# Kernel optimization log

Measured on AMD Instinct MI355X. Metric: run time of the kernel, lower is better.

The kernel has to match this reference:

```python
import jax, jax.numpy as jnp
import numpy as np

HEAD_DIM = 64

def setup_inputs() -> dict:
    key = jax.random.key(0)
    k1, k2, k3, k4, k5 = jax.random.split(key, 5)
    T, B, E = 2048, 4, 1024
    KD = 64  # kdim
    x = jax.random.normal(k1, (T, B, E), dtype=jnp.float32)
    in_proj_weight = jax.random.normal(k2, (3 * KD, HEAD_DIM), dtype=jnp.float32) * (1.0 / np.sqrt(HEAD_DIM))
    in_proj_bias = jnp.zeros((3 * KD,), dtype=jnp.float32)
    out_w = jax.random.normal(k4, (HEAD_DIM, KD), dtype=jnp.float32) * (1.0 / np.sqrt(KD))
    out_b = jnp.zeros((HEAD_DIM,), dtype=jnp.float32)
    return {"x": x, "in_proj_weight": in_proj_weight, "in_proj_bias": in_proj_bias,
            "out_w": out_w, "out_b": out_b}

def reference(x, in_proj_weight, in_proj_bias, out_w, out_b):
    # x: [T, B, E] with E = H * HEAD_DIM (qkv_same self-attention path)
    T, B, E = x.shape
    H = E // HEAD_DIM
    KD = in_proj_weight.shape[0] // 3
    scaling = HEAD_DIM ** (-0.5)
    # reshape splits embed dim into heads: [T, B*H, 64]
    xh = x.reshape(T, B * H, HEAD_DIM)
    # fused in-projection: [T, B*H, 3*KD], then chunk into q/k/v
    qkv = xh @ in_proj_weight.T + in_proj_bias
    q, k, v = jnp.split(qkv, 3, axis=-1)          # each [T, B*H, KD]
    q = q * scaling
    q = q.transpose(1, 0, 2)                      # [B*H, T, KD]
    k = k.transpose(1, 0, 2)
    v = v.transpose(1, 0, 2)
    scores = jnp.einsum('btd,bsd->bts', q, k)     # [B*H, T, T]
    w = jax.nn.softmax(scores, axis=-1)
    attn = jnp.einsum('bts,bsd->btd', w, v)       # [B*H, T, KD]
    attn = attn.transpose(1, 0, 2).reshape(T, B, H, KD)
    out = attn @ out_w.T + out_b                  # [T, B, H, HEAD_DIM]
    out = out.reshape(T, B, H * HEAD_DIM)         # [T, B, E]
    # averaged attention weights over heads: [B, T, T]
    avg_w = w.reshape(B, H, T, T).sum(axis=1) / H
    return out, avg_w
```

## Files before the change

kernel.cpp:

```cpp
#include <hip/hip_runtime.h>
#include <hip/hip_bf16.h>

#define T_DIM 2048
#define B_DIM 4
#define E_DIM 1024

typedef __bf16 bf16_t;
typedef bf16_t bf16x8 __attribute__((ext_vector_type(8)));
typedef float f32x16 __attribute__((ext_vector_type(16)));

union frag_u { uint4 u; bf16x8 b; };

constexpr float SCALEQ = 0.18033688011112042f;

__device__ __forceinline__ f32x16 mfma32(bf16x8 a, bf16x8 b, f32x16 c) {
  return __builtin_amdgcn_mfma_f32_32x32x16_bf16(a, b, c, 0, 0, 0);
}
__device__ __forceinline__ unsigned packbf(float a, float b) {
  union { bf16_t h[2]; unsigned u; } r;
  r.h[0] = (bf16_t)a; r.h[1] = (bf16_t)b; return r.u;
}
__device__ __forceinline__ void pl32swap(unsigned &x, unsigned &y) {
  asm volatile("v_permlane32_swap_b32 %0, %1" : "+v"(x), "+v"(y));
}
__device__ __forceinline__ void gload16(const void* g, void* l) {
  __builtin_amdgcn_global_load_lds((const __attribute__((address_space(1))) void*)g,
                                   (__attribute__((address_space(3))) void*)l, 16, 0, 0);
}
__device__ __forceinline__ bf16x8 ldc(const char* base, int chunk, int row) {
  frag_u f; f.u = *(const uint4*)(base + chunk * 1024 + row * 16); return f.b;
}
__device__ __forceinline__ float ex2(float x) { return __builtin_amdgcn_exp2f(x); }

#define VMCNT4 asm volatile("s_waitcnt vmcnt(4)" ::: "memory")
#define VMCNT0 asm volatile("s_waitcnt vmcnt(0)" ::: "memory")
#define LGKM0  asm volatile("s_waitcnt lgkmcnt(0)" ::: "memory")

template <int O>
__device__ __forceinline__ uint4 mkfrag(const f32x16& A) {
  unsigned X = packbf(A[O + 0], A[O + 1]);
  unsigned Z = packbf(A[O + 2], A[O + 3]);
  unsigned Y = packbf(A[O + 4], A[O + 5]);
  unsigned W = packbf(A[O + 6], A[O + 7]);
  pl32swap(X, Y); pl32swap(Z, W);
  return (uint4){X, Z, Y, W};
}

__global__ __launch_bounds__(256) void qkv_kernel(
    const float* __restrict__ x, const float* __restrict__ W,
    const float* __restrict__ bias,
    bf16_t* __restrict__ Qc, bf16_t* __restrict__ Kc, bf16_t* __restrict__ Vc) {
  __shared__ __align__(16) char xlds[16384];
  __shared__ __align__(16) char wlds[24576];
  __shared__ float bs[192];
  const int tid = threadIdx.x;
  const int bh = blockIdx.x >> 4;
  const int tt = blockIdx.x & 15;
  const int b = bh >> 4, h = bh & 15;
  const int t0 = tt * 128;
  const int wid = tid >> 6, lane = tid & 63;
  const int lq = lane & 31, hi = lane >> 5;

  for (int i = tid; i < 1024; i += 256) {
    int t = i >> 3, oct = i & 7;
    const float* src = x + ((size_t)(t0 + t) * B_DIM + b) * E_DIM + h * 64 + oct * 8;
    float4 f0 = *(const float4*)src;
    float4 f1 = *(const float4*)(src + 4);
    uint4 u;
    u.x = packbf(f0.x, f0.y); u.y = packbf(f0.z, f0.w);
    u.z = packbf(f1.x, f1.y); u.w = packbf(f1.z, f1.w);
    *(uint4*)(xlds + oct * 2048 + t * 16) = u;
  }
  for (int i = tid; i < 1536; i += 256) {
    int r = i >> 3, oct = i & 7;
    const float* src = W + r * 64 + oct * 8;
    float4 f0 = *(const float4*)src;
    float4 f1 = *(const float4*)(src + 4);
    uint4 u;
    u.x = packbf(f0.x, f0.y); u.y = packbf(f0.z, f0.w);
    u.z = packbf(f1.x, f1.y); u.w = packbf(f1.z, f1.w);
    *(uint4*)(wlds + oct * 3072 + r * 16) = u;
  }
  if (tid < 192) bs[tid] = bias[tid];
  __syncthreads();

  frag_u bx[4];
  #pragma unroll
  for (int s = 0; s < 4; ++s)
    bx[s].u = *(const uint4*)(xlds + (s * 2 + hi) * 2048 + (wid * 32 + lq) * 16);

  f32x16 acc[6];
  #pragma unroll
  for (int mt = 0; mt < 6; ++mt)
    #pragma unroll
    for (int r = 0; r < 16; ++r) acc[mt][r] = 0.f;

  #pragma unroll
  for (int mt = 0; mt < 6; ++mt) {
    #pragma unroll
    for (int s = 0; s < 4; ++s) {
      frag_u aw;
      aw.u = *(const uint4*)(wlds + (s * 2 + hi) * 3072 + (mt * 32 + lq) * 16);
      acc[mt] = mfma32(aw.b, bx[s].b, acc[mt]);
    }
  }

  const size_t tb = ((size_t)bh * 32 + (t0 >> 6) + (wid >> 1)) * 4096;
  const int trow = (wid & 1) * 32 + lq;

  #pragma unroll
  for (int mt = 0; mt < 6; ++mt) {
    #pragma unroll
    for (int g = 0; g < 4; ++g) {
      int rbase = mt * 32 + 8 * g + 4 * hi;
      float4 bq = *(const float4*)&bs[rbase];
      float v0 = acc[mt][4 * g + 0] + bq.x;
      float v1 = acc[mt][4 * g + 1] + bq.y;
      float v2 = acc[mt][4 * g + 2] + bq.z;
      float v3 = acc[mt][4 * g + 3] + bq.w;
      if (mt < 2) {
        union { ushort4 us; unsigned u2[2]; } pk;
        pk.u2[0] = packbf(v0 * SCALEQ, v1 * SCALEQ);
        pk.u2[1] = packbf(v2 * SCALEQ, v3 * SCALEQ);
        int d0 = rbase;
        *(ushort4*)(Qc + tb + (d0 >> 3) * 512 + trow * 8 + (d0 & 7)) = pk.us;
      } else if (mt < 4) {
        union { ushort4 us; unsigned u2[2]; } pk;
        pk.u2[0] = packbf(v0, v1);
        pk.u2[1] = packbf(v2, v3);
        int d0 = rbase - 64;
        *(ushort4*)(Kc + tb + (d0 >> 3) * 512 + trow * 8 + (d0 & 7)) = pk.us;
      } else {
        int d0 = rbase - 128;
        bf16_t* vdst = Vc + tb + (trow >> 3) * 512 + (trow & 7);
        vdst[(size_t)(d0 + 0) * 8] = (bf16_t)v0;
        vdst[(size_t)(d0 + 1) * 8] = (bf16_t)v1;
        vdst[(size_t)(d0 + 2) * 8] = (bf16_t)v2;
        vdst[(size_t)(d0 + 3) * 8] = (bf16_t)v3;
      }
    }
  }
}

__global__ __launch_bounds__(256, 2) void flash_kernel(
    const bf16_t* __restrict__ Qc, const bf16_t* __restrict__ Kc,
    const bf16_t* __restrict__ Vc,
    const float* __restrict__ Wo, const float* __restrict__ bo,
    float* __restrict__ out, float* __restrict__ Lv) {
  __shared__ __align__(16) char lds[32768];
  __shared__ __align__(16) char wlds[8192];
  const int tid = threadIdx.x;
  const int bid = ((blockIdx.x & 7) << 6) | (blockIdx.x >> 3);
  const int bh = bid >> 3, qb = bid & 7;
  const int b = bh >> 4, h = bh & 15;
  const int wid = tid >> 6, lane = tid & 63;
  const int lq = lane & 31, hi = lane >> 5;
  const int q0 = qb * 256 + wid * 64;

  for (int i = tid; i < 512; i += 256) {
    int d = i >> 3, oct = i & 7;
    const float* src = Wo + d * 64 + oct * 8;
    float4 f0 = *(const float4*)src;
    float4 f1 = *(const float4*)(src + 4);
    uint4 u;
    u.x = packbf(f0.x, f0.y); u.y = packbf(f0.z, f0.w);
    u.z = packbf(f1.x, f1.y); u.w = packbf(f1.z, f1.w);
    *(uint4*)(wlds + oct * 1024 + d * 16) = u;
  }

  const bf16_t* qtb = Qc + ((size_t)bh * 32 + (q0 >> 6)) * 4096;
  frag_u qfA[4], qfB[4];
  #pragma unroll
  for (int s = 0; s < 4; ++s) {
    qfA[s].u = *(const uint4*)(qtb + (s * 2 + hi) * 512 + lq * 8);
    qfB[s].u = *(const uint4*)(qtb + (s * 2 + hi) * 512 + (32 + lq) * 8);
  }

  f32x16 oA0, oA1, oB0, oB1;
  #pragma unroll
  for (int i = 0; i < 16; ++i) { oA0[i] = 0.f; oA1[i] = 0.f; oB0[i] = 0.f; oB1[i] = 0.f; }
  float lA = 0.f, lB = 0.f;

  const bf16_t* kbh = Kc + (size_t)bh * 131072;
  const bf16_t* vbh = Vc + (size_t)bh * 131072;
  auto stage = [&](int buf, int t) {
    char* kl_ = lds + buf * 16384 + wid * 2048;
    char* vl_ = kl_ + 8192;
    const bf16_t* kt = kbh + (size_t)t * 4096 + wid * 1024 + lane * 8;
    const bf16_t* vt = vbh + (size_t)t * 4096 + wid * 1024 + lane * 8;
    gload16(kt, kl_); gload16(kt + 512, kl_ + 1024);
    gload16(vt, vl_); gload16(vt + 512, vl_ + 1024);
  };

  stage(0, 0); stage(1, 1);
  VMCNT4; __builtin_amdgcn_sched_barrier(0);
  __builtin_amdgcn_s_barrier();

  for (int t = 0; t < 32; ++t) {
    const char* kl = lds + (t & 1) * 16384;
    const char* vl = kl + 8192;

    bf16x8 k0[4], k1[4];
    #pragma unroll
    for (int s = 0; s < 4; ++s) {
      k0[s] = ldc(kl, s * 2 + hi, lq);
      k1[s] = ldc(kl, s * 2 + hi, 32 + lq);
    }
    f32x16 aA0, aA1, aB0, aB1;
    #pragma unroll
    for (int i = 0; i < 16; ++i) { aA0[i] = 0.f; aA1[i] = 0.f; aB0[i] = 0.f; aB1[i] = 0.f; }
    __builtin_amdgcn_s_setprio(1);
    #pragma unroll
    for (int s = 0; s < 4; ++s) {
      aA0 = mfma32(k0[s], qfA[s].b, aA0);
      aA1 = mfma32(k1[s], qfA[s].b, aA1);
      aB0 = mfma32(k0[s], qfB[s].b, aB0);
      aB1 = mfma32(k1[s], qfB[s].b, aB1);
    }
    __builtin_amdgcn_s_setprio(0);

    bf16x8 v0[4], v1[4];
    #pragma unroll
    for (int s = 0; s < 4; ++s) {
      v0[s] = ldc(vl, s * 2 + hi, lq);
      v1[s] = ldc(vl, s * 2 + hi, 32 + lq);
    }
    LGKM0; __builtin_amdgcn_sched_barrier(0);
    __builtin_amdgcn_s_barrier();
    if (t + 2 < 32) stage(t & 1, t + 2);

    float lsA = 0.f, lsB = 0.f;
    #pragma unroll
    for (int i = 0; i < 16; ++i) {
      aA0[i] = ex2(aA0[i]); aA1[i] = ex2(aA1[i]);
      aB0[i] = ex2(aB0[i]); aB1[i] = ex2(aB1[i]);
      lsA += aA0[i] + aA1[i]; lsB += aB0[i] + aB1[i];
    }
    lA += lsA; lB += lsB;

    frag_u pA[4], pB[4];
    pA[0].u = mkfrag<0>(aA0); pA[1].u = mkfrag<8>(aA0);
    pA[2].u = mkfrag<0>(aA1); pA[3].u = mkfrag<8>(aA1);
    pB[0].u = mkfrag<0>(aB0); pB[1].u = mkfrag<8>(aB0);
    pB[2].u = mkfrag<0>(aB1); pB[3].u = mkfrag<8>(aB1);

    __builtin_amdgcn_s_setprio(1);
    #pragma unroll
    for (int ks = 0; ks < 4; ++ks) {
      oA0 = mfma32(v0[ks], pA[ks].b, oA0);
      oA1 = mfma32(v1[ks], pA[ks].b, oA1);
      oB0 = mfma32(v0[ks], pB[ks].b, oB0);
      oB1 = mfma32(v1[ks], pB[ks].b, oB1);
    }
    __builtin_amdgcn_s_setprio(0);

    if (t < 30) { VMCNT4; } else { VMCNT0; }
    __builtin_amdgcn_sched_barrier(0);
    __builtin_amdgcn_s_barrier();
  }

  float ltA = lA + __shfl_xor(lA, 32);
  float ltB = lB + __shfl_xor(lB, 32);
  float iA = 1.f / ltA, iB = 1.f / ltB;
  #pragma unroll
  for (int i = 0; i < 16; ++i) { oA0[i] *= iA; oA1[i] *= iA; oB0[i] *= iB; oB1[i] *= iB; }

  frag_u fA[4], fB[4];
  fA[0].u = mkfrag<0>(oA0); fA[1].u = mkfrag<8>(oA0);
  fA[2].u = mkfrag<0>(oA1); fA[3].u = mkfrag<8>(oA1);
  fB[0].u = mkfrag<0>(oB0); fB[1].u = mkfrag<8>(oB0);
  fB[2].u = mkfrag<0>(oB1); fB[3].u = mkfrag<8>(oB1);

  f32x16 cA0, cA1, cB0, cB1;
  #pragma unroll
  for (int i = 0; i < 16; ++i) { cA0[i] = 0.f; cA1[i] = 0.f; cB0[i] = 0.f; cB1[i] = 0.f; }
  #pragma unroll
  for (int s = 0; s < 4; ++s) {
    frag_u w0, w1;
    w0.u = *(const uint4*)(wlds + (s * 2 + hi) * 1024 + lq * 16);
    w1.u = *(const uint4*)(wlds + (s * 2 + hi) * 1024 + (32 + lq) * 16);
    cA0 = mfma32(fA[s].b, w0.b, cA0);
    cA1 = mfma32(fA[s].b, w1.b, cA1);
    cB0 = mfma32(fB[s].b, w0.b, cB0);
    cB1 = mfma32(fB[s].b, w1.b, cB1);
  }
  float bo0 = bo[lq], bo1 = bo[32 + lq];
  #pragma unroll
  for (int r = 0; r < 16; ++r) {
    int trA = q0 + (r & 3) + 8 * (r >> 2) + 4 * hi;
    int trB = trA + 32;
    out[((size_t)trA * B_DIM + b) * E_DIM + h * 64 + lq]      = cA0[r] + bo0;
    out[((size_t)trA * B_DIM + b) * E_DIM + h * 64 + 32 + lq] = cA1[r] + bo1;
    out[((size_t)trB * B_DIM + b) * E_DIM + h * 64 + lq]      = cB0[r] + bo0;
    out[((size_t)trB * B_DIM + b) * E_DIM + h * 64 + 32 + lq] = cB1[r] + bo1;
  }
  if (lane < 32) {
    Lv[(size_t)bh * T_DIM + q0 + lane] = ltA;
    Lv[(size_t)bh * T_DIM + q0 + 32 + lane] = ltB;
  }
}

__global__ __launch_bounds__(256, 2) void avgw_kernel(
    const bf16_t* __restrict__ Qc, const bf16_t* __restrict__ Kc,
    const float* __restrict__ Lv, float* __restrict__ avgw) {
  __shared__ __align__(16) char qlds[2][16384];
  __shared__ __align__(16) char klds[2][16384];
  __shared__ float lw[16][128];
  const int tid = threadIdx.x;
  const int bid = ((blockIdx.x & 7) << 7) | (blockIdx.x >> 3);
  const int b = bid >> 8, tq = (bid >> 4) & 15, sq = bid & 15;
  const int t0 = tq * 128, s0 = sq * 128;
  const int wid = tid >> 6, lane = tid & 63;
  const int lq = lane & 31, hi = lane >> 5;
  const int wr = wid >> 1, wc = wid & 1;

  for (int i = tid; i < 2048; i += 256) {
    int h = i >> 7, tt = i & 127;
    size_t idx = ((size_t)(b * 16 + h)) * T_DIM + t0 + tt;
    lw[h >> 3][0] = lw[h >> 3][0];
    lw[h][tt] = 1.0f / (16.0f * Lv[idx]);
  }

  auto stage = [&](int buf, int h) {
    int bh = b * 16 + h;
    const bf16_t* qt = Qc + ((size_t)bh * 32 + (t0 >> 6)) * 4096;
    const bf16_t* kt = Kc + ((size_t)bh * 32 + (s0 >> 6)) * 4096;
    #pragma unroll
    for (int j = 0; j < 4; ++j) {
      gload16(qt + wid * 2048 + j * 512 + lane * 8, qlds[buf] + wid * 4096 + j * 1024);
      gload16(kt + wid * 2048 + j * 512 + lane * 8, klds[buf] + wid * 4096 + j * 1024);
    }
  };

  f32x16 sacc[2][2];
  #pragma unroll
  for (int i = 0; i < 2; ++i)
    #pragma unroll
    for (int j = 0; j < 2; ++j)
      #pragma unroll
      for (int r = 0; r < 16; ++r) sacc[i][j][r] = 0.f;

  stage(0, 0);
  __syncthreads();

  for (int h = 0; h < 16; ++h) {
    if (h < 15) stage((h + 1) & 1, h + 1);
    const char* qb = qlds[h & 1];
    const char* kb = klds[h & 1];

    frag_u aq[2][4], ak[2][4];
    #pragma unroll
    for (int i = 0; i < 2; ++i)
      #pragma unroll
      for (int s = 0; s < 4; ++s) {
        int rq = wr * 64 + i * 32 + lq;
        int rk = wc * 64 + i * 32 + lq;
        aq[i][s].u = *(const uint4*)(qb + (rq >> 6) * 8192 + (s * 2 + hi) * 1024 + (rq & 63) * 16);
        ak[i][s].u = *(const uint4*)(kb + (rk >> 6) * 8192 + (s * 2 + hi) * 1024 + (rk & 63) * 16);
      }

    float lwr[2][16];
    #pragma unroll
    for (int i = 0; i < 2; ++i)
      #pragma unroll
      for (int r = 0; r < 16; ++r)
        lwr[i][r] = lw[h][wr * 64 + i * 32 + (r & 3) + ((r >> 2) << 3) + (hi << 2)];

    #pragma unroll
    for (int i = 0; i < 2; ++i)
      #pragma unroll
      for (int j = 0; j < 2; ++j) {
        f32x16 c;
        #pragma unroll
        for (int r = 0; r < 16; ++r) c[r] = 0.f;
        __builtin_amdgcn_s_setprio(1);
        #pragma unroll
        for (int s = 0; s < 4; ++s) c = mfma32(aq[i][s].b, ak[j][s].b, c);
        __builtin_amdgcn_s_setprio(0);
        #pragma unroll
        for (int r = 0; r < 16; ++r) sacc[i][j][r] += ex2(c[r]) * lwr[i][r];
      }
    __syncthreads();
  }

  #pragma unroll
  for (int i = 0; i < 2; ++i)
    #pragma unroll
    for (int j = 0; j < 2; ++j)
      #pragma unroll
      for (int r = 0; r < 16; ++r) {
        int trow = t0 + wr * 64 + i * 32 + (r & 3) + ((r >> 2) << 3) + (hi << 2);
        int scol = s0 + wc * 64 + j * 32 + lq;
        avgw[((size_t)b * T_DIM + trow) * T_DIM + scol] = sacc[i][j][r];
      }
}

extern "C" void kernel_launch(void* const* d_in, const int* in_sizes, int n_in,
                              void* d_out, int out_size, void* d_ws, size_t ws_size,
                              hipStream_t stream) {
  const float* x    = (const float*)d_in[0];
  const float* W    = (const float*)d_in[1];
  const float* bias = (const float*)d_in[2];
  const float* Wo   = (const float*)d_in[3];
  const float* bo   = (const float*)d_in[4];
  float* out  = (float*)d_out;
  float* avgw = out + (size_t)T_DIM * B_DIM * E_DIM;

  char* ws = (char*)d_ws;
  bf16_t* Qc = (bf16_t*)(ws);
  bf16_t* Kc = (bf16_t*)(ws + (16u << 20));
  bf16_t* Vc = (bf16_t*)(ws + (32u << 20));
  float*  Lv = (float*)(ws + (48u << 20));

  qkv_kernel<<<dim3(1024), dim3(256), 0, stream>>>(x, W, bias, Qc, Kc, Vc);
  flash_kernel<<<dim3(512), dim3(256), 0, stream>>>(Qc, Kc, Vc, Wo, bo, out, Lv);
  avgw_kernel<<<dim3(1024), dim3(256), 0, stream>>>(Qc, Kc, Lv, avgw);
}
```

Measured before the change: 178.2 us.

## Split flash attention KV sequence across waves with LDS reduction of partial outputs

The flash kernel now gives each block 64 queries instead of 256, and each of the four waves handles a quarter of the key/value sequence with its own private double-buffered LDS stage. Partial outputs and row sums are reduced through LDS, and the waves then split the output projection. This removes per-iteration block barriers and raises the grid from 512 to 2048 blocks for better occupancy and load balance. The cost is that every block rereads Wo, a larger LDS footprint (64KB) that may limit blocks per CU, and the extra reduction pass. MFMA chains now start from a zero constant instead of zeroing accumulators first.

```diff
diff --git a/kernel.cpp b/kernel.cpp
--- a/kernel.cpp
+++ b/kernel.cpp
@@ -7,6 +7,7 @@
 
 typedef __bf16 bf16_t;
 typedef bf16_t bf16x8 __attribute__((ext_vector_type(8)));
+typedef float f32x4 __attribute__((ext_vector_type(4)));
 typedef float f32x16 __attribute__((ext_vector_type(16)));
 
 union frag_u { uint4 u; bf16x8 b; };
@@ -27,14 +28,12 @@
   __builtin_amdgcn_global_load_lds((const __attribute__((address_space(1))) void*)g,
                                    (__attribute__((address_space(3))) void*)l, 16, 0, 0);
 }
-__device__ __forceinline__ bf16x8 ldc(const char* base, int chunk, int row) {
-  frag_u f; f.u = *(const uint4*)(base + chunk * 1024 + row * 16); return f.b;
-}
 __device__ __forceinline__ float ex2(float x) { return __builtin_amdgcn_exp2f(x); }
 
-#define VMCNT4 asm volatile("s_waitcnt vmcnt(4)" ::: "memory")
-#define VMCNT0 asm volatile("s_waitcnt vmcnt(0)" ::: "memory")
-#define LGKM0  asm volatile("s_waitcnt lgkmcnt(0)" ::: "memory")
+#define VMCNT8 do { asm volatile("s_waitcnt vmcnt(8)" ::: "memory"); \
+                    __builtin_amdgcn_sched_barrier(0); } while (0)
+#define VMCNT0 do { asm volatile("s_waitcnt vmcnt(0)" ::: "memory"); \
+                    __builtin_amdgcn_sched_barrier(0); } while (0)
 
 template <int O>
 __device__ __forceinline__ uint4 mkfrag(const f32x16& A) {
@@ -147,15 +146,16 @@
     const bf16_t* __restrict__ Vc,
     const float* __restrict__ Wo, const float* __restrict__ bo,
     float* __restrict__ out, float* __restrict__ Lv) {
-  __shared__ __align__(16) char lds[32768];
+  __shared__ __align__(16) char sbuf[65536];
   __shared__ __align__(16) char wlds[8192];
+  __shared__ float lbuf[4][64];
   const int tid = threadIdx.x;
-  const int bid = ((blockIdx.x & 7) << 6) | (blockIdx.x >> 3);
-  const int bh = bid >> 3, qb = bid & 7;
+  const int bid = ((blockIdx.x & 7) << 8) | (blockIdx.x >> 3);
+  const int bh = bid >> 5, qb = bid & 31;
   const int b = bh >> 4, h = bh & 15;
   const int wid = tid >> 6, lane = tid & 63;
   const int lq = lane & 31, hi = lane >> 5;
-  const int q0 = qb * 256 + wid * 64;
+  const int q0 = qb * 64;
 
   for (int i = tid; i < 512; i += 256) {
     int d = i >> 3, oct = i & 7;
@@ -176,127 +176,160 @@
     qfB[s].u = *(const uint4*)(qtb + (s * 2 + hi) * 512 + (32 + lq) * 8);
   }
 
-  f32x16 oA0, oA1, oB0, oB1;
-  #pragma unroll
-  for (int i = 0; i < 16; ++i) { oA0[i] = 0.f; oA1[i] = 0.f; oB0[i] = 0.f; oB1[i] = 0.f; }
-  float lA = 0.f, lB = 0.f;
+  f32x16 zc;
+  #pragma unroll
+  for (int i = 0; i < 16; ++i) zc[i] = 0.f;
+
+  f32x16 o00, o01, o10, o11;
+  #pragma unroll
+  for (int i = 0; i < 16; ++i) { o00[i] = 0.f; o01[i] = 0.f; o10[i] = 0.f; o11[i] = 0.f; }
+  float lAacc = 0.f, lBacc = 0.f;
 
   const bf16_t* kbh = Kc + (size_t)bh * 131072;
   const bf16_t* vbh = Vc + (size_t)bh * 131072;
+  const int koff = hi * 512 + lq * 8;
+  const int voff = lane * 8;
+  char* const myl = sbuf + wid * 16384;
+
   auto stage = [&](int buf, int t) {
-    char* kl_ = lds + buf * 16384 + wid * 2048;
-    char* vl_ = kl_ + 8192;
-    const bf16_t* kt = kbh + (size_t)t * 4096 + wid * 1024 + lane * 8;
-    const bf16_t* vt = vbh + (size_t)t * 4096 + wid * 1024 + lane * 8;
-    gload16(kt, kl_); gload16(kt + 512, kl_ + 1024);
-    gload16(vt, vl_); gload16(vt + 512, vl_ + 1024);
+    int kt = wid * 16 + t;
+    int tile = kt >> 1, half = kt & 1;
+    const bf16_t* kbt = kbh + (size_t)tile * 4096 + half * 256 + koff;
+    const bf16_t* vbt = vbh + (size_t)tile * 4096 + half * 2048 + voff;
+    char* kd = myl + buf * 8192;
+    char* vd = kd + 4096;
+    #pragma unroll
+    for (int j = 0; j < 4; ++j) {
+      gload16(kbt + j * 1024, kd + j * 1024);
+      gload16(vbt + j * 512, vd + j * 1024);
+    }
   };
 
-  stage(0, 0); stage(1, 1);
-  VMCNT4; __builtin_amdgcn_sched_barrier(0);
-  __builtin_amdgcn_s_barrier();
-
-  for (int t = 0; t < 32; ++t) {
-    const char* kl = lds + (t & 1) * 16384;
-    const char* vl = kl + 8192;
-
-    bf16x8 k0[4], k1[4];
+  stage(0, 0);
+
+  for (int t = 0; t < 16; ++t) {
+    const int cur = t & 1;
+    if (t < 15) { stage(cur ^ 1, t + 1); VMCNT8; } else { VMCNT0; }
+    const char* kl = myl + cur * 8192;
+    const char* vl = kl + 4096;
+
+    bf16x8 kf[4];
     #pragma unroll
     for (int s = 0; s < 4; ++s) {
-      k0[s] = ldc(kl, s * 2 + hi, lq);
-      k1[s] = ldc(kl, s * 2 + hi, 32 + lq);
-    }
-    f32x16 aA0, aA1, aB0, aB1;
-    #pragma unroll
-    for (int i = 0; i < 16; ++i) { aA0[i] = 0.f; aA1[i] = 0.f; aB0[i] = 0.f; aB1[i] = 0.f; }
+      frag_u f; f.u = *(const uint4*)(kl + (s * 2 + hi) * 512 + lq * 16);
+      kf[s] = f.b;
+    }
+    f32x16 aA, aB;
     __builtin_amdgcn_s_setprio(1);
-    #pragma unroll
-    for (int s = 0; s < 4; ++s) {
-      aA0 = mfma32(k0[s], qfA[s].b, aA0);
-      aA1 = mfma32(k1[s], qfA[s].b, aA1);
-      aB0 = mfma32(k0[s], qfB[s].b, aB0);
-      aB1 = mfma32(k1[s], qfB[s].b, aB1);
+    aA = mfma32(kf[0], qfA[0].b, zc);
+    aB = mfma32(kf[0], qfB[0].b, zc);
+    #pragma unroll
+    for (int s = 1; s < 4; ++s) {
+      aA = mfma32(kf[s], qfA[s].b, aA);
+      aB = mfma32(kf[s], qfB[s].b, aB);
     }
     __builtin_amdgcn_s_setprio(0);
 
-    bf16x8 v0[4], v1[4];
-    #pragma unroll
-    for (int s = 0; s < 4; ++s) {
-      v0[s] = ldc(vl, s * 2 + hi, lq);
-      v1[s] = ldc(vl, s * 2 + hi, 32 + lq);
-    }
-    LGKM0; __builtin_amdgcn_sched_barrier(0);
-    __builtin_amdgcn_s_barrier();
-    if (t + 2 < 32) stage(t & 1, t + 2);
-
-    float lsA = 0.f, lsB = 0.f;
-    #pragma unroll
-    for (int i = 0; i < 16; ++i) {
-      aA0[i] = ex2(aA0[i]); aA1[i] = ex2(aA1[i]);
-      aB0[i] = ex2(aB0[i]); aB1[i] = ex2(aB1[i]);
-      lsA += aA0[i] + aA1[i]; lsB += aB0[i] + aB1[i];
-    }
-    lA += lsA; lB += lsB;
-
-    frag_u pA[4], pB[4];
-    pA[0].u = mkfrag<0>(aA0); pA[1].u = mkfrag<8>(aA0);
-    pA[2].u = mkfrag<0>(aA1); pA[3].u = mkfrag<8>(aA1);
-    pB[0].u = mkfrag<0>(aB0); pB[1].u = mkfrag<8>(aB0);
-    pB[2].u = mkfrag<0>(aB1); pB[3].u = mkfrag<8>(aB1);
+    float sA0 = 0.f, sA1 = 0.f, sB0 = 0.f, sB1 = 0.f;
+    #pragma unroll
+    for (int i = 0; i < 8; ++i) {
+      aA[i] = ex2(aA[i]);     aA[i + 8] = ex2(aA[i + 8]);
+      aB[i] = ex2(aB[i]);     aB[i + 8] = ex2(aB[i + 8]);
+      sA0 += aA[i]; sA1 += aA[i + 8];
+      sB0 += aB[i]; sB1 += aB[i + 8];
+    }
+    lAacc += sA0 + sA1;
+    lBacc += sB0 + sB1;
+
+    frag_u pA0, pA1, pB0, pB1;
+    pA0.u = mkfrag<0>(aA); pA1.u = mkfrag<8>(aA);
+    pB0.u = mkfrag<0>(aB); pB1.u = mkfrag<8>(aB);
 
     __builtin_amdgcn_s_setprio(1);
-    #pragma unroll
-    for (int ks = 0; ks < 4; ++ks) {
-      oA0 = mfma32(v0[ks], pA[ks].b, oA0);
-      oA1 = mfma32(v1[ks], pA[ks].b, oA1);
-      oB0 = mfma32(v0[ks], pB[ks].b, oB0);
-      oB1 = mfma32(v1[ks], pB[ks].b, oB1);
+    {
+      frag_u v00, v01, v10, v11;
+      v00.u = *(const uint4*)(vl + (0 * 2 + hi) * 1024 + lq * 16);
+      v01.u = *(const uint4*)(vl + (0 * 2 + hi) * 1024 + (32 + lq) * 16);
+      v10.u = *(const uint4*)(vl + (1 * 2 + hi) * 1024 + lq * 16);
+      v11.u = *(const uint4*)(vl + (1 * 2 + hi) * 1024 + (32 + lq) * 16);
+      o00 = mfma32(v00.b, pA0.b, o00);
+      o01 = mfma32(v00.b, pB0.b, o01);
+      o10 = mfma32(v01.b, pA0.b, o10);
+      o11 = mfma32(v01.b, pB0.b, o11);
+      o00 = mfma32(v10.b, pA1.b, o00);
+      o01 = mfma32(v10.b, pB1.b, o01);
+      o10 = mfma32(v11.b, pA1.b, o10);
+      o11 = mfma32(v11.b, pB1.b, o11);
     }
     __builtin_amdgcn_s_setprio(0);
-
-    if (t < 30) { VMCNT4; } else { VMCNT0; }
-    __builtin_amdgcn_sched_barrier(0);
-    __builtin_amdgcn_s_barrier();
-  }
-
-  float ltA = lA + __shfl_xor(lA, 32);
-  float ltB = lB + __shfl_xor(lB, 32);
-  float iA = 1.f / ltA, iB = 1.f / ltB;
-  #pragma unroll
-  for (int i = 0; i < 16; ++i) { oA0[i] *= iA; oA1[i] *= iA; oB0[i] *= iB; oB1[i] *= iB; }
-
-  frag_u fA[4], fB[4];
-  fA[0].u = mkfrag<0>(oA0); fA[1].u = mkfrag<8>(oA0);
-  fA[2].u = mkfrag<0>(oA1); fA[3].u = mkfrag<8>(oA1);
-  fB[0].u = mkfrag<0>(oB0); fB[1].u = mkfrag<8>(oB0);
-  fB[2].u = mkfrag<0>(oB1); fB[3].u = mkfrag<8>(oB1);
-
-  f32x16 cA0, cA1, cB0, cB1;
-  #pragma unroll
-  for (int i = 0; i < 16; ++i) { cA0[i] = 0.f; cA1[i] = 0.f; cB0[i] = 0.f; cB1[i] = 0.f; }
+  }
+
+  float lA = lAacc + __shfl_xor(lAacc, 32);
+  float lB = lBacc + __shfl_xor(lBacc, 32);
+
+  {
+    #pragma unroll
+    for (int g = 0; g < 4; ++g) {
+      int ch = 2 * g + hi;
+      int qA = lq, qB = 32 + lq;
+      f32x4 w0, w1, w2, w3;
+      #pragma unroll
+      for (int e = 0; e < 4; ++e) {
+        w0[e] = o00[4 * g + e]; w1[e] = o10[4 * g + e];
+        w2[e] = o01[4 * g + e]; w3[e] = o11[4 * g + e];
+      }
+      *(f32x4*)(myl + qA * 256 + ((ch      ^ (qA & 15)) * 16)) = w0;
+      *(f32x4*)(myl + qA * 256 + (((ch + 8) ^ (qA & 15)) * 16)) = w1;
+      *(f32x4*)(myl + qB * 256 + ((ch      ^ (qB & 15)) * 16)) = w2;
+      *(f32x4*)(myl + qB * 256 + (((ch + 8) ^ (qB & 15)) * 16)) = w3;
+    }
+    if (lane < 32) {
+      lbuf[wid][lq] = lA;
+      lbuf[wid][32 + lq] = lB;
+    }
+  }
+  __syncthreads();
+
+  const int qsub = wid & 1, esub = wid >> 1;
+  const int q = qsub * 32 + lq;
+  float lt = lbuf[0][q] + lbuf[1][q] + lbuf[2][q] + lbuf[3][q];
+  float inv = 1.f / lt;
+  if (esub == 0 && lane < 32)
+    Lv[(size_t)bh * T_DIM + q0 + q] = lt;
+
+  frag_u fo[4];
   #pragma unroll
   for (int s = 0; s < 4; ++s) {
-    frag_u w0, w1;
-    w0.u = *(const uint4*)(wlds + (s * 2 + hi) * 1024 + lq * 16);
-    w1.u = *(const uint4*)(wlds + (s * 2 + hi) * 1024 + (32 + lq) * 16);
-    cA0 = mfma32(fA[s].b, w0.b, cA0);
-    cA1 = mfma32(fA[s].b, w1.b, cA1);
-    cB0 = mfma32(fB[s].b, w0.b, cB0);
-    cB1 = mfma32(fB[s].b, w1.b, cB1);
-  }
-  float bo0 = bo[lq], bo1 = bo[32 + lq];
+    int c0 = 4 * s + 2 * hi;
+    f32x4 u = {0.f, 0.f, 0.f, 0.f}, v = {0.f, 0.f, 0.f, 0.f};
+    #pragma unroll
+    for (int p = 0; p < 4; ++p) {
+      const char* pr = sbuf + p * 16384 + q * 256;
+      u += *(const f32x4*)(pr + ((c0      ^ (q & 15)) * 16));
+      v += *(const f32x4*)(pr + (((c0 + 1) ^ (q & 15)) * 16));
+    }
+    u *= inv; v *= inv;
+    fo[s].u = (uint4){packbf(u[0], u[1]), packbf(u[2], u[3]),
+                      packbf(v[0], v[1]), packbf(v[2], v[3])};
+  }
+
+  f32x16 cacc;
+  {
+    frag_u w0;
+    w0.u = *(const uint4*)(wlds + (0 * 2 + hi) * 1024 + (esub * 32 + lq) * 16);
+    cacc = mfma32(fo[0].b, w0.b, zc);
+    #pragma unroll
+    for (int s = 1; s < 4; ++s) {
+      frag_u ws;
+      ws.u = *(const uint4*)(wlds + (s * 2 + hi) * 1024 + (esub * 32 + lq) * 16);
+      cacc = mfma32(fo[s].b, ws.b, cacc);
+    }
+  }
+  float bov = bo[esub * 32 + lq];
   #pragma unroll
   for (int r = 0; r < 16; ++r) {
-    int trA = q0 + (r & 3) + 8 * (r >> 2) + 4 * hi;
-    int trB = trA + 32;
-    out[((size_t)trA * B_DIM + b) * E_DIM + h * 64 + lq]      = cA0[r] + bo0;
-    out[((size_t)trA * B_DIM + b) * E_DIM + h * 64 + 32 + lq] = cA1[r] + bo1;
-    out[((size_t)trB * B_DIM + b) * E_DIM + h * 64 + lq]      = cB0[r] + bo0;
-    out[((size_t)trB * B_DIM + b) * E_DIM + h * 64 + 32 + lq] = cB1[r] + bo1;
-  }
-  if (lane < 32) {
-    Lv[(size_t)bh * T_DIM + q0 + lane] = ltA;
-    Lv[(size_t)bh * T_DIM + q0 + 32 + lane] = ltB;
+    int trow = q0 + qsub * 32 + (r & 3) + 8 * (r >> 2) + 4 * hi;
+    out[((size_t)trow * B_DIM + b) * E_DIM + h * 64 + esub * 32 + lq] = cacc[r] + bov;
   }
 }
 
@@ -317,7 +350,6 @@
   for (int i = tid; i < 2048; i += 256) {
     int h = i >> 7, tt = i & 127;
     size_t idx = ((size_t)(b * 16 + h)) * T_DIM + t0 + tt;
-    lw[h >> 3][0] = lw[h >> 3][0];
     lw[h][tt] = 1.0f / (16.0f * Lv[idx]);
   }
 
@@ -331,6 +363,10 @@
       gload16(kt + wid * 2048 + j * 512 + lane * 8, klds[buf] + wid * 4096 + j * 1024);
     }
   };
+
+  f32x16 zc;
+  #pragma unroll
+  for (int r = 0; r < 16; ++r) zc[r] = 0.f;
 
   f32x16 sacc[2][2];
   #pragma unroll
@@ -370,12 +406,10 @@
     for (int i = 0; i < 2; ++i)
       #pragma unroll
       for (int j = 0; j < 2; ++j) {
-        f32x16 c;
+        __builtin_amdgcn_s_setprio(1);
+        f32x16 c = mfma32(aq[i][0].b, ak[j][0].b, zc);
         #pragma unroll
-        for (int r = 0; r < 16; ++r) c[r] = 0.f;
-        __builtin_amdgcn_s_setprio(1);
-        #pragma unroll
-        for (int s = 0; s < 4; ++s) c = mfma32(aq[i][s].b, ak[j][s].b, c);
+        for (int s = 1; s < 4; ++s) c = mfma32(aq[i][s].b, ak[j][s].b, c);
         __builtin_amdgcn_s_setprio(0);
         #pragma unroll
         for (int r = 0; r < 16; ++r) sacc[i][j][r] += ex2(c[r]) * lwr[i][r];
@@ -413,6 +447,6 @@
   float*  Lv = (float*)(ws + (48u << 20));
 
   qkv_kernel<<<dim3(1024), dim3(256), 0, stream>>>(x, W, bias, Qc, Kc, Vc);
-  flash_kernel<<<dim3(512), dim3(256), 0, stream>>>(Qc, Kc, Vc, Wo, bo, out, Lv);
+  flash_kernel<<<dim3(2048), dim3(256), 0, stream>>>(Qc, Kc, Vc, Wo, bo, out, Lv);
   avgw_kernel<<<dim3(1024), dim3(256), 0, stream>>>(Qc, Kc, Lv, avgw);
 }
```

Result: slower. 203.7 us (+14.3%).

## Split flash attention work across 8 waves of 32 query rows each

Applied to the files above, without the earlier changes.

The flash kernel now launches 512 threads per block, and each wave handles 32 query rows instead of 64. This halves the accumulator registers per wave so more waves can be resident, and the K/V staging is spread across 8 waves with one load each instead of four loads per wave. The avgw kernel reads the per-row softmax normalisers as vectorised float4 loads from LDS instead of building a 32-element register array, and both kernels start their first MFMA from a shared zero constant. The trade-off is that each wave now reuses every K/V fragment read from LDS for half as many query rows, which raises LDS traffic.

```diff
diff --git a/kernel.cpp b/kernel.cpp
--- a/kernel.cpp
+++ b/kernel.cpp
@@ -7,6 +7,7 @@
 
 typedef __bf16 bf16_t;
 typedef bf16_t bf16x8 __attribute__((ext_vector_type(8)));
+typedef float f32x4 __attribute__((ext_vector_type(4)));
 typedef float f32x16 __attribute__((ext_vector_type(16)));
 
 union frag_u { uint4 u; bf16x8 b; };
@@ -32,9 +33,12 @@
 }
 __device__ __forceinline__ float ex2(float x) { return __builtin_amdgcn_exp2f(x); }
 
-#define VMCNT4 asm volatile("s_waitcnt vmcnt(4)" ::: "memory")
-#define VMCNT0 asm volatile("s_waitcnt vmcnt(0)" ::: "memory")
-#define LGKM0  asm volatile("s_waitcnt lgkmcnt(0)" ::: "memory")
+#define VMCNT2 do { asm volatile("s_waitcnt vmcnt(2)" ::: "memory"); \
+                    __builtin_amdgcn_sched_barrier(0); } while (0)
+#define VMCNT0 do { asm volatile("s_waitcnt vmcnt(0)" ::: "memory"); \
+                    __builtin_amdgcn_sched_barrier(0); } while (0)
+#define LGKM0  do { asm volatile("s_waitcnt lgkmcnt(0)" ::: "memory"); \
+                    __builtin_amdgcn_sched_barrier(0); } while (0)
 
 template <int O>
 __device__ __forceinline__ uint4 mkfrag(const f32x16& A) {
@@ -142,7 +146,7 @@
   }
 }
 
-__global__ __launch_bounds__(256, 2) void flash_kernel(
+__global__ __launch_bounds__(512, 4) void flash_kernel(
     const bf16_t* __restrict__ Qc, const bf16_t* __restrict__ Kc,
     const bf16_t* __restrict__ Vc,
     const float* __restrict__ Wo, const float* __restrict__ bo,
@@ -155,46 +159,46 @@
   const int b = bh >> 4, h = bh & 15;
   const int wid = tid >> 6, lane = tid & 63;
   const int lq = lane & 31, hi = lane >> 5;
-  const int q0 = qb * 256 + wid * 64;
-
-  for (int i = tid; i < 512; i += 256) {
-    int d = i >> 3, oct = i & 7;
-    const float* src = Wo + d * 64 + oct * 8;
+  const int qw = qb * 256 + wid * 32;
+
+  {
+    const float* src = Wo + (tid >> 3) * 64 + (tid & 7) * 8;
     float4 f0 = *(const float4*)src;
     float4 f1 = *(const float4*)(src + 4);
     uint4 u;
     u.x = packbf(f0.x, f0.y); u.y = packbf(f0.z, f0.w);
     u.z = packbf(f1.x, f1.y); u.w = packbf(f1.z, f1.w);
-    *(uint4*)(wlds + oct * 1024 + d * 16) = u;
-  }
-
-  const bf16_t* qtb = Qc + ((size_t)bh * 32 + (q0 >> 6)) * 4096;
-  frag_u qfA[4], qfB[4];
-  #pragma unroll
-  for (int s = 0; s < 4; ++s) {
-    qfA[s].u = *(const uint4*)(qtb + (s * 2 + hi) * 512 + lq * 8);
-    qfB[s].u = *(const uint4*)(qtb + (s * 2 + hi) * 512 + (32 + lq) * 8);
-  }
-
-  f32x16 oA0, oA1, oB0, oB1;
-  #pragma unroll
-  for (int i = 0; i < 16; ++i) { oA0[i] = 0.f; oA1[i] = 0.f; oB0[i] = 0.f; oB1[i] = 0.f; }
-  float lA = 0.f, lB = 0.f;
+    *(uint4*)(wlds + (tid & 7) * 1024 + (tid >> 3) * 16) = u;
+  }
+
+  const bf16_t* qtb = Qc + ((size_t)bh * 32 + (qw >> 6)) * 4096;
+  const int qrow = qw & 63;
+  frag_u qf[4];
+  #pragma unroll
+  for (int s = 0; s < 4; ++s)
+    qf[s].u = *(const uint4*)(qtb + (s * 2 + hi) * 512 + (qrow + lq) * 8);
+
+  f32x16 zc;
+  #pragma unroll
+  for (int i = 0; i < 16; ++i) zc[i] = 0.f;
+
+  f32x16 o0, o1;
+  #pragma unroll
+  for (int i = 0; i < 16; ++i) { o0[i] = 0.f; o1[i] = 0.f; }
+  float lacc = 0.f;
 
   const bf16_t* kbh = Kc + (size_t)bh * 131072;
   const bf16_t* vbh = Vc + (size_t)bh * 131072;
   auto stage = [&](int buf, int t) {
-    char* kl_ = lds + buf * 16384 + wid * 2048;
-    char* vl_ = kl_ + 8192;
-    const bf16_t* kt = kbh + (size_t)t * 4096 + wid * 1024 + lane * 8;
-    const bf16_t* vt = vbh + (size_t)t * 4096 + wid * 1024 + lane * 8;
-    gload16(kt, kl_); gload16(kt + 512, kl_ + 1024);
-    gload16(vt, vl_); gload16(vt + 512, vl_ + 1024);
+    char* kd = lds + buf * 16384;
+    const bf16_t* kt = kbh + (size_t)t * 4096 + wid * 512 + lane * 8;
+    const bf16_t* vt = vbh + (size_t)t * 4096 + wid * 512 + lane * 8;
+    gload16(kt, kd + wid * 1024);
+    gload16(vt, kd + 8192 + wid * 1024);
   };
 
   stage(0, 0); stage(1, 1);
-  VMCNT4; __builtin_amdgcn_sched_barrier(0);
-  __builtin_amdgcn_s_barrier();
+  __syncthreads();
 
   for (int t = 0; t < 32; ++t) {
     const char* kl = lds + (t & 1) * 16384;
@@ -206,98 +210,83 @@
       k0[s] = ldc(kl, s * 2 + hi, lq);
       k1[s] = ldc(kl, s * 2 + hi, 32 + lq);
     }
-    f32x16 aA0, aA1, aB0, aB1;
-    #pragma unroll
-    for (int i = 0; i < 16; ++i) { aA0[i] = 0.f; aA1[i] = 0.f; aB0[i] = 0.f; aB1[i] = 0.f; }
+    f32x16 a0, a1;
     __builtin_amdgcn_s_setprio(1);
-    #pragma unroll
-    for (int s = 0; s < 4; ++s) {
-      aA0 = mfma32(k0[s], qfA[s].b, aA0);
-      aA1 = mfma32(k1[s], qfA[s].b, aA1);
-      aB0 = mfma32(k0[s], qfB[s].b, aB0);
-      aB1 = mfma32(k1[s], qfB[s].b, aB1);
+    a0 = mfma32(k0[0], qf[0].b, zc);
+    a1 = mfma32(k1[0], qf[0].b, zc);
+    #pragma unroll
+    for (int s = 1; s < 4; ++s) {
+      a0 = mfma32(k0[s], qf[s].b, a0);
+      a1 = mfma32(k1[s], qf[s].b, a1);
     }
     __builtin_amdgcn_s_setprio(0);
 
     bf16x8 v0[4], v1[4];
     #pragma unroll
-    for (int s = 0; s < 4; ++s) {
-      v0[s] = ldc(vl, s * 2 + hi, lq);
-      v1[s] = ldc(vl, s * 2 + hi, 32 + lq);
-    }
-    LGKM0; __builtin_amdgcn_sched_barrier(0);
+    for (int ks = 0; ks < 4; ++ks) {
+      v0[ks] = ldc(vl, ks * 2 + hi, lq);
+      v1[ks] = ldc(vl, ks * 2 + hi, 32 + lq);
+    }
+    LGKM0;
     __builtin_amdgcn_s_barrier();
     if (t + 2 < 32) stage(t & 1, t + 2);
 
-    float lsA = 0.f, lsB = 0.f;
+    float s0 = 0.f, s1 = 0.f;
     #pragma unroll
     for (int i = 0; i < 16; ++i) {
-      aA0[i] = ex2(aA0[i]); aA1[i] = ex2(aA1[i]);
-      aB0[i] = ex2(aB0[i]); aB1[i] = ex2(aB1[i]);
-      lsA += aA0[i] + aA1[i]; lsB += aB0[i] + aB1[i];
-    }
-    lA += lsA; lB += lsB;
-
-    frag_u pA[4], pB[4];
-    pA[0].u = mkfrag<0>(aA0); pA[1].u = mkfrag<8>(aA0);
-    pA[2].u = mkfrag<0>(aA1); pA[3].u = mkfrag<8>(aA1);
-    pB[0].u = mkfrag<0>(aB0); pB[1].u = mkfrag<8>(aB0);
-    pB[2].u = mkfrag<0>(aB1); pB[3].u = mkfrag<8>(aB1);
+      a0[i] = ex2(a0[i]); s0 += a0[i];
+      a1[i] = ex2(a1[i]); s1 += a1[i];
+    }
+    lacc += s0 + s1;
+
+    frag_u p0, p1, p2, p3;
+    p0.u = mkfrag<0>(a0); p1.u = mkfrag<8>(a0);
+    p2.u = mkfrag<0>(a1); p3.u = mkfrag<8>(a1);
 
     __builtin_amdgcn_s_setprio(1);
-    #pragma unroll
-    for (int ks = 0; ks < 4; ++ks) {
-      oA0 = mfma32(v0[ks], pA[ks].b, oA0);
-      oA1 = mfma32(v1[ks], pA[ks].b, oA1);
-      oB0 = mfma32(v0[ks], pB[ks].b, oB0);
-      oB1 = mfma32(v1[ks], pB[ks].b, oB1);
-    }
+    o0 = mfma32(v0[0], p0.b, o0); o1 = mfma32(v1[0], p0.b, o1);
+    o0 = mfma32(v0[1], p1.b, o0); o1 = mfma32(v1[1], p1.b, o1);
+    o0 = mfma32(v0[2], p2.b, o0); o1 = mfma32(v1[2], p2.b, o1);
+    o0 = mfma32(v0[3], p3.b, o0); o1 = mfma32(v1[3], p3.b, o1);
     __builtin_amdgcn_s_setprio(0);
 
-    if (t < 30) { VMCNT4; } else { VMCNT0; }
-    __builtin_amdgcn_sched_barrier(0);
+    if (t < 30) { VMCNT2; } else { VMCNT0; }
     __builtin_amdgcn_s_barrier();
   }
 
-  float ltA = lA + __shfl_xor(lA, 32);
-  float ltB = lB + __shfl_xor(lB, 32);
-  float iA = 1.f / ltA, iB = 1.f / ltB;
-  #pragma unroll
-  for (int i = 0; i < 16; ++i) { oA0[i] *= iA; oA1[i] *= iA; oB0[i] *= iB; oB1[i] *= iB; }
-
-  frag_u fA[4], fB[4];
-  fA[0].u = mkfrag<0>(oA0); fA[1].u = mkfrag<8>(oA0);
-  fA[2].u = mkfrag<0>(oA1); fA[3].u = mkfrag<8>(oA1);
-  fB[0].u = mkfrag<0>(oB0); fB[1].u = mkfrag<8>(oB0);
-  fB[2].u = mkfrag<0>(oB1); fB[3].u = mkfrag<8>(oB1);
-
-  f32x16 cA0, cA1, cB0, cB1;
-  #pragma unroll
-  for (int i = 0; i < 16; ++i) { cA0[i] = 0.f; cA1[i] = 0.f; cB0[i] = 0.f; cB1[i] = 0.f; }
-  #pragma unroll
-  for (int s = 0; s < 4; ++s) {
+  float lt = lacc + __shfl_xor(lacc, 32);
+  float inv = 1.f / lt;
+  #pragma unroll
+  for (int i = 0; i < 16; ++i) { o0[i] *= inv; o1[i] *= inv; }
+
+  frag_u fo[4];
+  fo[0].u = mkfrag<0>(o0); fo[1].u = mkfrag<8>(o0);
+  fo[2].u = mkfrag<0>(o1); fo[3].u = mkfrag<8>(o1);
+
+  f32x16 c0, c1;
+  {
     frag_u w0, w1;
-    w0.u = *(const uint4*)(wlds + (s * 2 + hi) * 1024 + lq * 16);
-    w1.u = *(const uint4*)(wlds + (s * 2 + hi) * 1024 + (32 + lq) * 16);
-    cA0 = mfma32(fA[s].b, w0.b, cA0);
-    cA1 = mfma32(fA[s].b, w1.b, cA1);
-    cB0 = mfma32(fB[s].b, w0.b, cB0);
-    cB1 = mfma32(fB[s].b, w1.b, cB1);
+    w0.u = *(const uint4*)(wlds + (0 * 2 + hi) * 1024 + lq * 16);
+    w1.u = *(const uint4*)(wlds + (0 * 2 + hi) * 1024 + (32 + lq) * 16);
+    c0 = mfma32(fo[0].b, w0.b, zc);
+    c1 = mfma32(fo[0].b, w1.b, zc);
+    #pragma unroll
+    for (int s = 1; s < 4; ++s) {
+      w0.u = *(const uint4*)(wlds + (s * 2 + hi) * 1024 + lq * 16);
+      w1.u = *(const uint4*)(wlds + (s * 2 + hi) * 1024 + (32 + lq) * 16);
+      c0 = mfma32(fo[s].b, w0.b, c0);
+      c1 = mfma32(fo[s].b, w1.b, c1);
+    }
   }
   float bo0 = bo[lq], bo1 = bo[32 + lq];
   #pragma unroll
   for (int r = 0; r < 16; ++r) {
-    int trA = q0 + (r & 3) + 8 * (r >> 2) + 4 * hi;
-    int trB = trA + 32;
-    out[((size_t)trA * B_DIM + b) * E_DIM + h * 64 + lq]      = cA0[r] + bo0;
-    out[((size_t)trA * B_DIM + b) * E_DIM + h * 64 + 32 + lq] = cA1[r] + bo1;
-    out[((size_t)trB * B_DIM + b) * E_DIM + h * 64 + lq]      = cB0[r] + bo0;
-    out[((size_t)trB * B_DIM + b) * E_DIM + h * 64 + 32 + lq] = cB1[r] + bo1;
-  }
-  if (lane < 32) {
-    Lv[(size_t)bh * T_DIM + q0 + lane] = ltA;
-    Lv[(size_t)bh * T_DIM + q0 + 32 + lane] = ltB;
-  }
+    int tr = qw + (r & 3) + 8 * (r >> 2) + 4 * hi;
+    out[((size_t)tr * B_DIM + b) * E_DIM + h * 64 + lq]      = c0[r] + bo0;
+    out[((size_t)tr * B_DIM + b) * E_DIM + h * 64 + 32 + lq] = c1[r] + bo1;
+  }
+  if (lane < 32)
+    Lv[(size_t)bh * T_DIM + qw + lq] = lt;
 }
 
 __global__ __launch_bounds__(256, 2) void avgw_kernel(
@@ -317,7 +306,6 @@
   for (int i = tid; i < 2048; i += 256) {
     int h = i >> 7, tt = i & 127;
     size_t idx = ((size_t)(b * 16 + h)) * T_DIM + t0 + tt;
-    lw[h >> 3][0] = lw[h >> 3][0];
     lw[h][tt] = 1.0f / (16.0f * Lv[idx]);
   }
 
@@ -331,6 +319,10 @@
       gload16(kt + wid * 2048 + j * 512 + lane * 8, klds[buf] + wid * 4096 + j * 1024);
     }
   };
+
+  f32x16 zc;
+  #pragma unroll
+  for (int r = 0; r < 16; ++r) zc[r] = 0.f;
 
   f32x16 sacc[2][2];
   #pragma unroll
@@ -359,26 +351,22 @@
         ak[i][s].u = *(const uint4*)(kb + (rk >> 6) * 8192 + (s * 2 + hi) * 1024 + (rk & 63) * 16);
       }
 
-    float lwr[2][16];
-    #pragma unroll
-    for (int i = 0; i < 2; ++i)
-      #pragma unroll
-      for (int r = 0; r < 16; ++r)
-        lwr[i][r] = lw[h][wr * 64 + i * 32 + (r & 3) + ((r >> 2) << 3) + (hi << 2)];
-
     #pragma unroll
     for (int i = 0; i < 2; ++i)
       #pragma unroll
       for (int j = 0; j < 2; ++j) {
-        f32x16 c;
+        __builtin_amdgcn_s_setprio(1);
+        f32x16 c = mfma32(aq[i][0].b, ak[j][0].b, zc);
         #pragma unroll
-        for (int r = 0; r < 16; ++r) c[r] = 0.f;
-        __builtin_amdgcn_s_setprio(1);
-        #pragma unroll
-        for (int s = 0; s < 4; ++s) c = mfma32(aq[i][s].b, ak[j][s].b, c);
+        for (int s = 1; s < 4; ++s) c = mfma32(aq[i][s].b, ak[j][s].b, c);
         __builtin_amdgcn_s_setprio(0);
         #pragma unroll
-        for (int r = 0; r < 16; ++r) sacc[i][j][r] += ex2(c[r]) * lwr[i][r];
+        for (int g = 0; g < 4; ++g) {
+          f32x4 l4 = *(const f32x4*)&lw[h][wr * 64 + i * 32 + 8 * g + 4 * hi];
+          #pragma unroll
+          for (int e = 0; e < 4; ++e)
+            sacc[i][j][4 * g + e] += ex2(c[4 * g + e]) * l4[e];
+        }
       }
     __syncthreads();
   }
@@ -413,6 +401,6 @@
   float*  Lv = (float*)(ws + (48u << 20));
 
   qkv_kernel<<<dim3(1024), dim3(256), 0, stream>>>(x, W, bias, Qc, Kc, Vc);
-  flash_kernel<<<dim3(512), dim3(256), 0, stream>>>(Qc, Kc, Vc, Wo, bo, out, Lv);
+  flash_kernel<<<dim3(512), dim3(512), 0, stream>>>(Qc, Kc, Vc, Wo, bo, out, Lv);
   avgw_kernel<<<dim3(1024), dim3(256), 0, stream>>>(Qc, Kc, Lv, avgw);
 }
```

Result: slower. 183.2 us (+2.8%).
